# Optimization experiments

Hardware: AMD Instinct MI355X
Metric: run time of the kernel (lower is better)

## Reference

```python
import jax, jax.numpy as jnp
import numpy as np

N = 300000        # active voxels
C = 64            # channels (in_dim == out_dim)
K = 27            # 3x3x3 kernel offsets
EPS = 1e-5        # BatchNorm eps
GX, GY, GZ = 256, 256, 32  # voxel grid


def _build_neighbors():
    """Submanifold rulebook: for each active voxel, index of the active voxel at
    each of the 27 offsets, or -1 if that neighbor voxel is inactive."""
    rng = np.random.default_rng(0)
    lin = np.sort(rng.choice(GX * GY * GZ, size=N, replace=False))
    x, y, z = lin // (GY * GZ), (lin // GZ) % GY, lin % GZ
    nbr = np.full((N, K), -1, dtype=np.int32)
    k = 0
    for dx in (-1, 0, 1):
        for dy in (-1, 0, 1):
            for dz in (-1, 0, 1):
                nx, ny, nz = x + dx, y + dy, z + dz
                inb = (nx >= 0) & (nx < GX) & (ny >= 0) & (ny < GY) & (nz >= 0) & (nz < GZ)
                nl = (nx * GY + ny) * GZ + nz
                pos = np.searchsorted(lin, nl)
                posc = np.clip(pos, 0, N - 1)
                found = inb & (lin[posc] == nl)
                nbr[:, k] = np.where(found, posc, -1)
                k += 1
    return jnp.asarray(nbr)


def setup_inputs() -> dict:
    key = jax.random.key(0)
    k0, k1, k2 = jax.random.split(key, 3)
    return {
        "feats": jax.random.normal(k0, (N, C), dtype=jnp.float32),
        "W1": jax.random.normal(k1, (K, C, C), dtype=jnp.float32) * 0.05,
        "gamma1": jnp.ones((C,), jnp.float32),
        "beta1": jnp.zeros((C,), jnp.float32),
        "W2": jax.random.normal(k2, (K, C, C), dtype=jnp.float32) * 0.05,
        "gamma2": jnp.ones((C,), jnp.float32),
        "beta2": jnp.zeros((C,), jnp.float32),
        "neighbor_idx": _build_neighbors(),
    }


def _subm_conv(feats, W, nbr):
    # gather -> matmul -> accumulate, one pass per kernel offset (fixed K=27)
    mask = nbr >= 0
    idx = jnp.where(mask, nbr, 0)
    out = jnp.zeros((feats.shape[0], W.shape[-1]), feats.dtype)
    for k in range(K):
        g = feats[idx[:, k]] * mask[:, k:k + 1].astype(feats.dtype)  # [N, C]
        out = out + g @ W[k]
    return out


def _bn_relu(x, gamma, beta):
    # BatchNorm1d training-mode forward: biased batch stats over active voxels
    mu = jnp.mean(x, axis=0)
    var = jnp.var(x, axis=0)
    return jax.nn.relu((x - mu) * jax.lax.rsqrt(var + EPS) * gamma + beta)


def reference(feats, W1, gamma1, beta1, W2, gamma2, beta2, neighbor_idx):
    x_net = _bn_relu(_subm_conv(feats, W1, neighbor_idx), gamma1, beta1)
    res = _bn_relu(_subm_conv(x_net, W2, neighbor_idx), gamma2, beta2)
    return x_net + res
```

## Files before the change

### kernel.cpp

```cpp
#include <hip/hip_runtime.h>
#include <cstdint>
#include <cstddef>

typedef unsigned short u16;
typedef __bf16 bf16x8 __attribute__((ext_vector_type(8)));
typedef float f32x4 __attribute__((ext_vector_type(4)));

#define KOFF 27
#define EPSBN 1e-5f

__device__ inline u16 f2bf(float f) {
  unsigned int u = __float_as_uint(f);
  unsigned int r = (u + 0x7FFFu + ((u >> 16) & 1u)) >> 16;
  return (u16)r;
}
__device__ inline float bf2f(u16 h) {
  return __uint_as_float(((unsigned int)h) << 16);
}


__global__ void k_prep_feats(const float* __restrict__ in, u16* __restrict__ out,
                             float* __restrict__ stats, int n4) {
  if (blockIdx.x == 0) stats[threadIdx.x] = 0.f;
  int i = blockIdx.x * 256 + threadIdx.x;
  if (i >= n4) return;
  const float4 v = reinterpret_cast<const float4*>(in)[i];
  ushort4 o;
  o.x = f2bf(v.x); o.y = f2bf(v.y); o.z = f2bf(v.z); o.w = f2bf(v.w);
  reinterpret_cast<ushort4*>(out)[i] = o;
}

__global__ void k_prep_w(const float* __restrict__ W, u16* __restrict__ Wp) {
  int tid = blockIdx.x * 256 + threadIdx.x;
  if (tid >= KOFF * 4096) return;
  int k = tid >> 12;
  int rem = tid & 4095;
  int slot = rem >> 3;
  int e = rem & 7;
  int ks = slot >> 8;
  int ct = (slot >> 6) & 3;
  int lane = slot & 63;
  int j = ks * 32 + ((lane >> 4) << 3) + e;
  int c = ct * 16 + (lane & 15);
  Wp[tid] = f2bf(W[(k * 64 + j) * 64 + c]);
}

__global__ void k_prep_nbrT(const int* __restrict__ nbr, int* __restrict__ nbrT, int N) {
  __shared__ int L[64 * KOFF];
  const int t = threadIdx.x;
  const int v0 = blockIdx.x * 64;
  const int nv = min(64, N - v0);
  const int cnt = nv * KOFF;
  for (int i = t; i < cnt; i += 256) L[i] = nbr[(size_t)v0 * KOFF + i];
  __syncthreads();
  for (int i = t; i < KOFF * 64; i += 256) {
    int k = i >> 6, j = i & 63;
    if (j < nv) nbrT[(size_t)k * N + v0 + j] = L[j * KOFF + k];
  }
}

__launch_bounds__(256, 3)
__global__ void k_conv(const u16* __restrict__ F, const u16* __restrict__ Wp,
                       const int* __restrict__ nbrT, float* __restrict__ out,
                       float* __restrict__ stats, int N) {
  const int t = threadIdx.x;
  const int w = t >> 6;
  const int lane = t & 63;
  const int vbase = blockIdx.x * 256 + (w << 6) + (lane & 15);
  const int ch = (lane >> 4) << 3;

  f32x4 acc[4][4];
#pragma unroll
  for (int m = 0; m < 4; ++m)
#pragma unroll
    for (int c = 0; c < 4; ++c) acc[m][c] = (f32x4){0.f, 0.f, 0.f, 0.f};

  int nid[4];
#pragma unroll
  for (int m = 0; m < 4; ++m) {
    const int v = vbase + (m << 4);
    nid[m] = (v < N) ? nbrT[v] : -1;
  }

  const u16* bp = Wp + ((size_t)lane << 3);

#pragma unroll 3
  for (int k = 0; k < KOFF; ++k) {
    bf16x8 bfr[2][4];
#pragma unroll
    for (int ks = 0; ks < 2; ++ks)
#pragma unroll
      for (int c = 0; c < 4; ++c)
        bfr[ks][c] = *reinterpret_cast<const bf16x8*>(bp + ((size_t)k << 12) + (ks << 11) + (c << 9));

    bf16x8 a0[4], a1[4];
#pragma unroll
    for (int m = 0; m < 4; ++m) {
      a0[m] = (bf16x8){};
      a1[m] = (bf16x8){};
      const int id = nid[m];
      if (id >= 0) {
        const u16* fr = F + ((size_t)id << 6) + ch;
        a0[m] = *reinterpret_cast<const bf16x8*>(fr);
        a1[m] = *reinterpret_cast<const bf16x8*>(fr + 32);
      }
    }

    if (k + 1 < KOFF) {
      const int* nk = nbrT + (size_t)(k + 1) * N;
#pragma unroll
      for (int m = 0; m < 4; ++m) {
        const int v = vbase + (m << 4);
        nid[m] = (v < N) ? nk[v] : -1;
      }
    }

#pragma unroll
    for (int m = 0; m < 4; ++m)
#pragma unroll
      for (int c = 0; c < 4; ++c)
        acc[m][c] = __builtin_amdgcn_mfma_f32_16x16x32_bf16(a0[m], bfr[0][c], acc[m][c], 0, 0, 0);
#pragma unroll
    for (int m = 0; m < 4; ++m)
#pragma unroll
      for (int c = 0; c < 4; ++c)
        acc[m][c] = __builtin_amdgcn_mfma_f32_16x16x32_bf16(a1[m], bfr[1][c], acc[m][c], 0, 0, 0);
  }

  const int row0 = blockIdx.x * 256 + (w << 6) + ((lane >> 4) << 2);
#pragma unroll
  for (int m = 0; m < 4; ++m) {
#pragma unroll
    for (int c = 0; c < 4; ++c) {
      const int col = (c << 4) + (lane & 15);
#pragma unroll
      for (int e = 0; e < 4; ++e) {
        const int v = row0 + (m << 4) + e;
        if (v < N) out[((size_t)v << 6) + col] = acc[m][c][e];
      }
    }
  }

  __shared__ float sred[4][128];
#pragma unroll
  for (int c = 0; c < 4; ++c) {
    float s = 0.f, q = 0.f;
#pragma unroll
    for (int m = 0; m < 4; ++m)
#pragma unroll
      for (int e = 0; e < 4; ++e) {
        const float x = acc[m][c][e];
        s += x;
        q += x * x;
      }
    s += __shfl_xor(s, 16, 64);
    s += __shfl_xor(s, 32, 64);
    q += __shfl_xor(q, 16, 64);
    q += __shfl_xor(q, 32, 64);
    if (lane < 16) {
      sred[w][(c << 4) + lane] = s;
      sred[w][64 + (c << 4) + lane] = q;
    }
  }
  __syncthreads();
  if (t < 128) {
    const float tot = sred[0][t] + sred[1][t] + sred[2][t] + sred[3][t];
    atomicAdd(&stats[t], tot);
  }
}


__global__ void k_final(const float* __restrict__ stats, const float* __restrict__ gamma,
                        const float* __restrict__ beta, float* __restrict__ sb, int N) {
  const int c = threadIdx.x;
  const float inv = 1.0f / (float)N;
  const float mu = stats[c] * inv;
  const float var = stats[64 + c] * inv - mu * mu;
  const float sc = gamma[c] * rsqrtf(var + EPSBN);
  sb[c] = sc;
  sb[64 + c] = beta[c] - mu * sc;
}

__global__ void k_apply1(const float* __restrict__ x, const float* __restrict__ sb,
                         u16* __restrict__ xb, int n4) {
  int i = blockIdx.x * 256 + threadIdx.x;
  if (i >= n4) return;
  const int cg = i & 15;
  float4 v = reinterpret_cast<const float4*>(x)[i];
  const float4 sc = reinterpret_cast<const float4*>(sb)[cg];
  const float4 bi = reinterpret_cast<const float4*>(sb)[16 + cg];
  float y0 = fmaxf(0.f, v.x * sc.x + bi.x);
  float y1 = fmaxf(0.f, v.y * sc.y + bi.y);
  float y2 = fmaxf(0.f, v.z * sc.z + bi.z);
  float y3 = fmaxf(0.f, v.w * sc.w + bi.w);
  ushort4 o;
  o.x = f2bf(y0); o.y = f2bf(y1); o.z = f2bf(y2); o.w = f2bf(y3);
  reinterpret_cast<ushort4*>(xb)[i] = o;
}

__global__ void k_apply2(float* __restrict__ io, const float* __restrict__ sb,
                         const u16* __restrict__ xb, int n4) {
  int i = blockIdx.x * 256 + threadIdx.x;
  if (i >= n4) return;
  const int cg = i & 15;
  float4 v = reinterpret_cast<const float4*>(io)[i];
  const float4 sc = reinterpret_cast<const float4*>(sb)[cg];
  const float4 bi = reinterpret_cast<const float4*>(sb)[16 + cg];
  const ushort4 xn = reinterpret_cast<const ushort4*>(xb)[i];
  float4 o;
  o.x = bf2f(xn.x) + fmaxf(0.f, v.x * sc.x + bi.x);
  o.y = bf2f(xn.y) + fmaxf(0.f, v.y * sc.y + bi.y);
  o.z = bf2f(xn.z) + fmaxf(0.f, v.z * sc.z + bi.z);
  o.w = bf2f(xn.w) + fmaxf(0.f, v.w * sc.w + bi.w);
  reinterpret_cast<float4*>(io)[i] = o;
}


extern "C" void kernel_launch(void* const* d_in, const int* in_sizes, int n_in,
                              void* d_out, int out_size, void* d_ws, size_t ws_size,
                              hipStream_t stream) {
  const float* feats = (const float*)d_in[0];
  const float* W1 = (const float*)d_in[1];
  const float* g1 = (const float*)d_in[2];
  const float* b1 = (const float*)d_in[3];
  const float* W2 = (const float*)d_in[4];
  const float* g2 = (const float*)d_in[5];
  const float* b2 = (const float*)d_in[6];
  const int* nbr = (const int*)d_in[7];
  const int N = in_sizes[0] / 64;

  char* ws = (char*)d_ws;
  size_t off = 0;
  auto alloc = [&](size_t bytes) {
    void* p = ws + off;
    off = (off + bytes + 255) & ~(size_t)255;
    return p;
  };
  u16* featsb = (u16*)alloc((size_t)N * 64 * 2);
  u16* xnetb = (u16*)alloc((size_t)N * 64 * 2);
  u16* w1p = (u16*)alloc((size_t)KOFF * 4096 * 2);
  u16* w2p = (u16*)alloc((size_t)KOFF * 4096 * 2);
  float* stats = (float*)alloc(256 * 4);
  float* sb1 = (float*)alloc(128 * 4);
  float* sb2 = (float*)alloc(128 * 4);
  int* nbrT = (int*)alloc((size_t)KOFF * N * 4);
  float* outf = (float*)d_out;

  const int n4 = N * 16;
  const int gApply = (n4 + 255) / 256;
  const int gW = (KOFF * 4096 + 255) / 256;
  const int gConv = (N + 255) / 256;

  k_prep_feats<<<gApply, 256, 0, stream>>>(feats, featsb, stats, n4);
  k_prep_w<<<gW, 256, 0, stream>>>(W1, w1p);
  k_prep_w<<<gW, 256, 0, stream>>>(W2, w2p);
  k_prep_nbrT<<<(N + 63) / 64, 256, 0, stream>>>(nbr, nbrT, N);

  k_conv<<<gConv, 256, 0, stream>>>(featsb, w1p, nbrT, outf, stats, N);
  k_final<<<1, 64, 0, stream>>>(stats, g1, b1, sb1, N);
  k_apply1<<<gApply, 256, 0, stream>>>(outf, sb1, xnetb, n4);

  k_conv<<<gConv, 256, 0, stream>>>(xnetb, w2p, nbrT, outf, stats + 128, N);
  k_final<<<1, 64, 0, stream>>>(stats + 128, g2, b2, sb2, N);
  k_apply2<<<gApply, 256, 0, stream>>>(outf, sb2, xnetb, n4);
}
```

Baseline: 267.4 us.

## Double-buffer conv gathers, remap blocks per XCD, store raw conv outputs as bf16

The conv kernel now prefetches the next offset's neighbor features and weight fragments into a second register set while MFMAs run on the current set. It also skips MFMAs for 16-row groups whose neighbors are all missing, raises MFMA priority with s_setprio, and remaps block IDs so consecutive voxel tiles share an XCD's L2. Raw conv outputs are written as bf16 instead of fp32, which halves the write and re-read traffic in the apply kernels. The apply kernels are widened to 8 elements per thread. The costs are higher register pressure (occupancy hint lowered from 3 to 2) and extra bf16 rounding of the pre-BatchNorm values.

New measurement: 368.1 us. 1.38x slower.

```diff
diff --git a/kernel.cpp b/kernel.cpp
--- a/kernel.cpp
+++ b/kernel.cpp
@@ -59,15 +59,70 @@
   }
 }
 
-__launch_bounds__(256, 3)
+
+__device__ __forceinline__ void conv_step(
+    const u16* __restrict__ F, const u16* __restrict__ bp,
+    const int* __restrict__ nbrT, int N, int vbase, const bool (&vok)[4],
+    int kk, int chb,
+    bf16x8 (&c0)[4], bf16x8 (&c1)[4], bf16x8 (&cb)[2][4], bool (&cball)[4],
+    bf16x8 (&n0)[4], bf16x8 (&n1)[4], bf16x8 (&nb)[2][4], bool (&nball)[4],
+    int (&nid)[4], f32x4 (&acc)[4][4]) {
+  const int kn = kk + 1;
+  if (kn < KOFF) {
+#pragma unroll
+    for (int m = 0; m < 4; ++m) {
+      const int id = nid[m];
+      nball[m] = __any(id >= 0);
+      n0[m] = (bf16x8){};
+      n1[m] = (bf16x8){};
+      if (id >= 0) {
+        const char* fr = (const char*)F + ((size_t)(unsigned)id << 7) + chb;
+        n0[m] = *reinterpret_cast<const bf16x8*>(fr);
+        n1[m] = *reinterpret_cast<const bf16x8*>(fr + 64);
+      }
+    }
+    if (kn + 1 < KOFF) {
+      const int* nk = nbrT + (size_t)(kn + 1) * N + vbase;
+#pragma unroll
+      for (int m = 0; m < 4; ++m) nid[m] = vok[m] ? nk[m << 4] : -1;
+    }
+    const u16* bk = bp + ((size_t)kn << 12);
+#pragma unroll
+    for (int ks = 0; ks < 2; ++ks)
+#pragma unroll
+      for (int c = 0; c < 4; ++c)
+        nb[ks][c] = *reinterpret_cast<const bf16x8*>(bk + (ks << 11) + (c << 9));
+  }
+  __builtin_amdgcn_s_setprio(1);
+#pragma unroll
+  for (int m = 0; m < 4; ++m) {
+    if (cball[m]) {
+#pragma unroll
+      for (int c = 0; c < 4; ++c)
+        acc[m][c] = __builtin_amdgcn_mfma_f32_16x16x32_bf16(c0[m], cb[0][c], acc[m][c], 0, 0, 0);
+#pragma unroll
+      for (int c = 0; c < 4; ++c)
+        acc[m][c] = __builtin_amdgcn_mfma_f32_16x16x32_bf16(c1[m], cb[1][c], acc[m][c], 0, 0, 0);
+    }
+  }
+  __builtin_amdgcn_s_setprio(0);
+}
+
+__launch_bounds__(256, 2)
 __global__ void k_conv(const u16* __restrict__ F, const u16* __restrict__ Wp,
-                       const int* __restrict__ nbrT, float* __restrict__ out,
+                       const int* __restrict__ nbrT, u16* __restrict__ rawout,
                        float* __restrict__ stats, int N) {
   const int t = threadIdx.x;
   const int w = t >> 6;
   const int lane = t & 63;
-  const int vbase = blockIdx.x * 256 + (w << 6) + (lane & 15);
-  const int ch = (lane >> 4) << 3;
+
+  const int nwg = gridDim.x, bid = blockIdx.x;
+  const int q = nwg >> 3, r = nwg & 7;
+  const int xcd = bid & 7, o = bid >> 3;
+  const int wg = (xcd < r ? xcd * (q + 1) : r * (q + 1) + (xcd - r) * q) + o;
+
+  const int vbase = wg * 256 + (w << 6) + (lane & 15);
+  const int chb = (lane >> 4) << 4;
 
   f32x4 acc[4][4];
 #pragma unroll
@@ -75,59 +130,53 @@
 #pragma unroll
     for (int c = 0; c < 4; ++c) acc[m][c] = (f32x4){0.f, 0.f, 0.f, 0.f};
 
+  bool vok[4];
   int nid[4];
 #pragma unroll
   for (int m = 0; m < 4; ++m) {
     const int v = vbase + (m << 4);
-    nid[m] = (v < N) ? nbrT[v] : -1;
-  }
-
-  const u16* bp = Wp + ((size_t)lane << 3);
-
-#pragma unroll 3
-  for (int k = 0; k < KOFF; ++k) {
-    bf16x8 bfr[2][4];
-#pragma unroll
-    for (int ks = 0; ks < 2; ++ks)
-#pragma unroll
-      for (int c = 0; c < 4; ++c)
-        bfr[ks][c] = *reinterpret_cast<const bf16x8*>(bp + ((size_t)k << 12) + (ks << 11) + (c << 9));
-
-    bf16x8 a0[4], a1[4];
-#pragma unroll
-    for (int m = 0; m < 4; ++m) {
-      a0[m] = (bf16x8){};
-      a1[m] = (bf16x8){};
-      const int id = nid[m];
-      if (id >= 0) {
-        const u16* fr = F + ((size_t)id << 6) + ch;
-        a0[m] = *reinterpret_cast<const bf16x8*>(fr);
-        a1[m] = *reinterpret_cast<const bf16x8*>(fr + 32);
-      }
-    }
-
-    if (k + 1 < KOFF) {
-      const int* nk = nbrT + (size_t)(k + 1) * N;
-#pragma unroll
-      for (int m = 0; m < 4; ++m) {
-        const int v = vbase + (m << 4);
-        nid[m] = (v < N) ? nk[v] : -1;
-      }
-    }
-
-#pragma unroll
-    for (int m = 0; m < 4; ++m)
-#pragma unroll
-      for (int c = 0; c < 4; ++c)
-        acc[m][c] = __builtin_amdgcn_mfma_f32_16x16x32_bf16(a0[m], bfr[0][c], acc[m][c], 0, 0, 0);
-#pragma unroll
-    for (int m = 0; m < 4; ++m)
-#pragma unroll
-      for (int c = 0; c < 4; ++c)
-        acc[m][c] = __builtin_amdgcn_mfma_f32_16x16x32_bf16(a1[m], bfr[1][c], acc[m][c], 0, 0, 0);
-  }
-
-  const int row0 = blockIdx.x * 256 + (w << 6) + ((lane >> 4) << 2);
+    vok[m] = v < N;
+    nid[m] = vok[m] ? nbrT[v] : -1;
+  }
+
+  bf16x8 a0A[4], a1A[4], bA[2][4];
+  bf16x8 a0B[4], a1B[4], bB[2][4];
+  bool ballA[4], ballB[4];
+
+#pragma unroll
+  for (int m = 0; m < 4; ++m) {
+    const int id = nid[m];
+    ballA[m] = __any(id >= 0);
+    a0A[m] = (bf16x8){};
+    a1A[m] = (bf16x8){};
+    if (id >= 0) {
+      const char* fr = (const char*)F + ((size_t)(unsigned)id << 7) + chb;
+      a0A[m] = *reinterpret_cast<const bf16x8*>(fr);
+      a1A[m] = *reinterpret_cast<const bf16x8*>(fr + 64);
+    }
+  }
+  {
+    const int* nk = nbrT + (size_t)N + vbase;
+#pragma unroll
+    for (int m = 0; m < 4; ++m) nid[m] = vok[m] ? nk[m << 4] : -1;
+  }
+  const u16* bp = Wp + (lane << 3);
+#pragma unroll
+  for (int ks = 0; ks < 2; ++ks)
+#pragma unroll
+    for (int c = 0; c < 4; ++c)
+      bA[ks][c] = *reinterpret_cast<const bf16x8*>(bp + (ks << 11) + (c << 9));
+
+  for (int kb = 0; kb < 13; ++kb) {
+    conv_step(F, bp, nbrT, N, vbase, vok, 2 * kb, chb,
+              a0A, a1A, bA, ballA, a0B, a1B, bB, ballB, nid, acc);
+    conv_step(F, bp, nbrT, N, vbase, vok, 2 * kb + 1, chb,
+              a0B, a1B, bB, ballB, a0A, a1A, bA, ballA, nid, acc);
+  }
+  conv_step(F, bp, nbrT, N, vbase, vok, 26, chb,
+            a0A, a1A, bA, ballA, a0B, a1B, bB, ballB, nid, acc);
+
+  const int row0 = wg * 256 + (w << 6) + ((lane >> 4) << 2);
 #pragma unroll
   for (int m = 0; m < 4; ++m) {
 #pragma unroll
@@ -136,7 +185,7 @@
 #pragma unroll
       for (int e = 0; e < 4; ++e) {
         const int v = row0 + (m << 4) + e;
-        if (v < N) out[((size_t)v << 6) + col] = acc[m][c][e];
+        if (v < N) rawout[((size_t)v << 6) + col] = f2bf(acc[m][c][e]);
       }
     }
   }
@@ -144,22 +193,22 @@
   __shared__ float sred[4][128];
 #pragma unroll
   for (int c = 0; c < 4; ++c) {
-    float s = 0.f, q = 0.f;
+    float s = 0.f, qq = 0.f;
 #pragma unroll
     for (int m = 0; m < 4; ++m)
 #pragma unroll
       for (int e = 0; e < 4; ++e) {
         const float x = acc[m][c][e];
         s += x;
-        q += x * x;
+        qq += x * x;
       }
     s += __shfl_xor(s, 16, 64);
     s += __shfl_xor(s, 32, 64);
-    q += __shfl_xor(q, 16, 64);
-    q += __shfl_xor(q, 32, 64);
+    qq += __shfl_xor(qq, 16, 64);
+    qq += __shfl_xor(qq, 32, 64);
     if (lane < 16) {
       sred[w][(c << 4) + lane] = s;
-      sred[w][64 + (c << 4) + lane] = q;
+      sred[w][64 + (c << 4) + lane] = qq;
     }
   }
   __syncthreads();
@@ -181,38 +230,58 @@
   sb[64 + c] = beta[c] - mu * sc;
 }
 
-__global__ void k_apply1(const float* __restrict__ x, const float* __restrict__ sb,
-                         u16* __restrict__ xb, int n4) {
+__global__ void k_apply1(const u16* __restrict__ raw, const float* __restrict__ sb,
+                         u16* __restrict__ xb, int n8) {
   int i = blockIdx.x * 256 + threadIdx.x;
-  if (i >= n4) return;
-  const int cg = i & 15;
-  float4 v = reinterpret_cast<const float4*>(x)[i];
-  const float4 sc = reinterpret_cast<const float4*>(sb)[cg];
-  const float4 bi = reinterpret_cast<const float4*>(sb)[16 + cg];
-  float y0 = fmaxf(0.f, v.x * sc.x + bi.x);
-  float y1 = fmaxf(0.f, v.y * sc.y + bi.y);
-  float y2 = fmaxf(0.f, v.z * sc.z + bi.z);
-  float y3 = fmaxf(0.f, v.w * sc.w + bi.w);
-  ushort4 o;
-  o.x = f2bf(y0); o.y = f2bf(y1); o.z = f2bf(y2); o.w = f2bf(y3);
-  reinterpret_cast<ushort4*>(xb)[i] = o;
-}
-
-__global__ void k_apply2(float* __restrict__ io, const float* __restrict__ sb,
-                         const u16* __restrict__ xb, int n4) {
+  if (i >= n8) return;
+  const int cg = (i & 7) << 1;
+  const uint4 rv = reinterpret_cast<const uint4*>(raw)[i];
+  const float4 s0 = reinterpret_cast<const float4*>(sb)[cg];
+  const float4 s1 = reinterpret_cast<const float4*>(sb)[cg + 1];
+  const float4 b0 = reinterpret_cast<const float4*>(sb + 64)[cg];
+  const float4 b1 = reinterpret_cast<const float4*>(sb + 64)[cg + 1];
+  uint4 ov;
+  {
+    float y0 = fmaxf(0.f, bf2f((u16)(rv.x & 0xffff)) * s0.x + b0.x);
+    float y1 = fmaxf(0.f, bf2f((u16)(rv.x >> 16)) * s0.y + b0.y);
+    float y2 = fmaxf(0.f, bf2f((u16)(rv.y & 0xffff)) * s0.z + b0.z);
+    float y3 = fmaxf(0.f, bf2f((u16)(rv.y >> 16)) * s0.w + b0.w);
+    ov.x = (unsigned)f2bf(y0) | ((unsigned)f2bf(y1) << 16);
+    ov.y = (unsigned)f2bf(y2) | ((unsigned)f2bf(y3) << 16);
+  }
+  {
+    float y0 = fmaxf(0.f, bf2f((u16)(rv.z & 0xffff)) * s1.x + b1.x);
+    float y1 = fmaxf(0.f, bf2f((u16)(rv.z >> 16)) * s1.y + b1.y);
+    float y2 = fmaxf(0.f, bf2f((u16)(rv.w & 0xffff)) * s1.z + b1.z);
+    float y3 = fmaxf(0.f, bf2f((u16)(rv.w >> 16)) * s1.w + b1.w);
+    ov.z = (unsigned)f2bf(y0) | ((unsigned)f2bf(y1) << 16);
+    ov.w = (unsigned)f2bf(y2) | ((unsigned)f2bf(y3) << 16);
+  }
+  reinterpret_cast<uint4*>(xb)[i] = ov;
+}
+
+__global__ void k_apply2(const u16* __restrict__ raw, const float* __restrict__ sb,
+                         const u16* __restrict__ xb, float* __restrict__ out, int n8) {
   int i = blockIdx.x * 256 + threadIdx.x;
-  if (i >= n4) return;
-  const int cg = i & 15;
-  float4 v = reinterpret_cast<const float4*>(io)[i];
-  const float4 sc = reinterpret_cast<const float4*>(sb)[cg];
-  const float4 bi = reinterpret_cast<const float4*>(sb)[16 + cg];
-  const ushort4 xn = reinterpret_cast<const ushort4*>(xb)[i];
-  float4 o;
-  o.x = bf2f(xn.x) + fmaxf(0.f, v.x * sc.x + bi.x);
-  o.y = bf2f(xn.y) + fmaxf(0.f, v.y * sc.y + bi.y);
-  o.z = bf2f(xn.z) + fmaxf(0.f, v.z * sc.z + bi.z);
-  o.w = bf2f(xn.w) + fmaxf(0.f, v.w * sc.w + bi.w);
-  reinterpret_cast<float4*>(io)[i] = o;
+  if (i >= n8) return;
+  const int cg = (i & 7) << 1;
+  const uint4 rv = reinterpret_cast<const uint4*>(raw)[i];
+  const uint4 xv = reinterpret_cast<const uint4*>(xb)[i];
+  const float4 s0 = reinterpret_cast<const float4*>(sb)[cg];
+  const float4 s1 = reinterpret_cast<const float4*>(sb)[cg + 1];
+  const float4 b0 = reinterpret_cast<const float4*>(sb + 64)[cg];
+  const float4 b1 = reinterpret_cast<const float4*>(sb + 64)[cg + 1];
+  float4 o0, o1;
+  o0.x = bf2f((u16)(xv.x & 0xffff)) + fmaxf(0.f, bf2f((u16)(rv.x & 0xffff)) * s0.x + b0.x);
+  o0.y = bf2f((u16)(xv.x >> 16)) + fmaxf(0.f, bf2f((u16)(rv.x >> 16)) * s0.y + b0.y);
+  o0.z = bf2f((u16)(xv.y & 0xffff)) + fmaxf(0.f, bf2f((u16)(rv.y & 0xffff)) * s0.z + b0.z);
+  o0.w = bf2f((u16)(xv.y >> 16)) + fmaxf(0.f, bf2f((u16)(rv.y >> 16)) * s0.w + b0.w);
+  o1.x = bf2f((u16)(xv.z & 0xffff)) + fmaxf(0.f, bf2f((u16)(rv.z & 0xffff)) * s1.x + b1.x);
+  o1.y = bf2f((u16)(xv.z >> 16)) + fmaxf(0.f, bf2f((u16)(rv.z >> 16)) * s1.y + b1.y);
+  o1.z = bf2f((u16)(xv.w & 0xffff)) + fmaxf(0.f, bf2f((u16)(rv.w & 0xffff)) * s1.z + b1.z);
+  o1.w = bf2f((u16)(xv.w >> 16)) + fmaxf(0.f, bf2f((u16)(rv.w >> 16)) * s1.w + b1.w);
+  reinterpret_cast<float4*>(out)[2 * i] = o0;
+  reinterpret_cast<float4*>(out)[2 * i + 1] = o1;
 }
 
 
@@ -244,23 +313,28 @@
   float* sb1 = (float*)alloc(128 * 4);
   float* sb2 = (float*)alloc(128 * 4);
   int* nbrT = (int*)alloc((size_t)KOFF * N * 4);
+
+  u16* raw1 = (u16*)d_out;
+  u16* raw2 = featsb;
   float* outf = (float*)d_out;
 
   const int n4 = N * 16;
-  const int gApply = (n4 + 255) / 256;
+  const int n8 = N * 8;
+  const int gPrep = (n4 + 255) / 256;
+  const int gApply = (n8 + 255) / 256;
   const int gW = (KOFF * 4096 + 255) / 256;
   const int gConv = (N + 255) / 256;
 
-  k_prep_feats<<<gApply, 256, 0, stream>>>(feats, featsb, stats, n4);
+  k_prep_feats<<<gPrep, 256, 0, stream>>>(feats, featsb, stats, n4);
   k_prep_w<<<gW, 256, 0, stream>>>(W1, w1p);
   k_prep_w<<<gW, 256, 0, stream>>>(W2, w2p);
   k_prep_nbrT<<<(N + 63) / 64, 256, 0, stream>>>(nbr, nbrT, N);
 
-  k_conv<<<gConv, 256, 0, stream>>>(featsb, w1p, nbrT, outf, stats, N);
+  k_conv<<<gConv, 256, 0, stream>>>(featsb, w1p, nbrT, raw1, stats, N);
   k_final<<<1, 64, 0, stream>>>(stats, g1, b1, sb1, N);
-  k_apply1<<<gApply, 256, 0, stream>>>(outf, sb1, xnetb, n4);
-
-  k_conv<<<gConv, 256, 0, stream>>>(xnetb, w2p, nbrT, outf, stats + 128, N);
+  k_apply1<<<gApply, 256, 0, stream>>>(raw1, sb1, xnetb, n8);
+
+  k_conv<<<gConv, 256, 0, stream>>>(xnetb, w2p, nbrT, raw2, stats + 128, N);
   k_final<<<1, 64, 0, stream>>>(stats + 128, g2, b2, sb2, N);
-  k_apply2<<<gApply, 256, 0, stream>>>(outf, sb2, xnetb, n4);
-}
+  k_apply2<<<gApply, 256, 0, stream>>>(raw2, sb2, xnetb, outf, n8);
+}
```

## Halve conv tile per block, raise occupancy, remap blocks across XCDs

Applied to the files above, without the earlier changes.

The conv kernel now processes 128 voxels per block instead of 256, with 2 M-tiles per wave instead of 4. This cuts accumulator registers and allows 4 blocks per SIMD set via launch bounds. Block IDs are remapped so that consecutive voxel ranges land on the same XCD, which should improve L2 locality for neighbor gathers. The cost is that each B-fragment weight load is reused across fewer MFMAs, raising weight-load traffic per voxel.

After: 324.8 us. 1.21x slower.

```diff
diff --git a/kernel.cpp b/kernel.cpp
--- a/kernel.cpp
+++ b/kernel.cpp
@@ -59,30 +59,38 @@
   }
 }
 
-__launch_bounds__(256, 3)
+__launch_bounds__(256, 4)
 __global__ void k_conv(const u16* __restrict__ F, const u16* __restrict__ Wp,
                        const int* __restrict__ nbrT, float* __restrict__ out,
                        float* __restrict__ stats, int N) {
   const int t = threadIdx.x;
   const int w = t >> 6;
   const int lane = t & 63;
-  const int vbase = blockIdx.x * 256 + (w << 6) + (lane & 15);
+
+  const int nwg = gridDim.x, bid = blockIdx.x;
+  const int q = nwg >> 3, r = nwg & 7;
+  const int xcd = bid & 7, o = bid >> 3;
+  const int wg = (xcd < r ? xcd * (q + 1) : r * (q + 1) + (xcd - r) * q) + o;
+
+  const int vbase = wg * 128 + (w << 5) + (lane & 15);
   const int ch = (lane >> 4) << 3;
 
-  f32x4 acc[4][4];
-#pragma unroll
-  for (int m = 0; m < 4; ++m)
+  f32x4 acc[2][4];
+#pragma unroll
+  for (int m = 0; m < 2; ++m)
 #pragma unroll
     for (int c = 0; c < 4; ++c) acc[m][c] = (f32x4){0.f, 0.f, 0.f, 0.f};
 
-  int nid[4];
-#pragma unroll
-  for (int m = 0; m < 4; ++m) {
+  bool vok[2];
+  int nid[2];
+#pragma unroll
+  for (int m = 0; m < 2; ++m) {
     const int v = vbase + (m << 4);
-    nid[m] = (v < N) ? nbrT[v] : -1;
-  }
-
-  const u16* bp = Wp + ((size_t)lane << 3);
+    vok[m] = v < N;
+    nid[m] = vok[m] ? nbrT[v] : -1;
+  }
+
+  const u16* bp = Wp + (lane << 3);
 
 #pragma unroll 3
   for (int k = 0; k < KOFF; ++k) {
@@ -93,14 +101,14 @@
       for (int c = 0; c < 4; ++c)
         bfr[ks][c] = *reinterpret_cast<const bf16x8*>(bp + ((size_t)k << 12) + (ks << 11) + (c << 9));
 
-    bf16x8 a0[4], a1[4];
-#pragma unroll
-    for (int m = 0; m < 4; ++m) {
+    bf16x8 a0[2], a1[2];
+#pragma unroll
+    for (int m = 0; m < 2; ++m) {
       a0[m] = (bf16x8){};
       a1[m] = (bf16x8){};
       const int id = nid[m];
       if (id >= 0) {
-        const u16* fr = F + ((size_t)id << 6) + ch;
+        const u16* fr = F + ((size_t)(unsigned)id << 6) + ch;
         a0[m] = *reinterpret_cast<const bf16x8*>(fr);
         a1[m] = *reinterpret_cast<const bf16x8*>(fr + 32);
       }
@@ -109,27 +117,27 @@
     if (k + 1 < KOFF) {
       const int* nk = nbrT + (size_t)(k + 1) * N;
 #pragma unroll
-      for (int m = 0; m < 4; ++m) {
+      for (int m = 0; m < 2; ++m) {
         const int v = vbase + (m << 4);
         nid[m] = (v < N) ? nk[v] : -1;
       }
     }
 
 #pragma unroll
-    for (int m = 0; m < 4; ++m)
+    for (int m = 0; m < 2; ++m)
 #pragma unroll
       for (int c = 0; c < 4; ++c)
         acc[m][c] = __builtin_amdgcn_mfma_f32_16x16x32_bf16(a0[m], bfr[0][c], acc[m][c], 0, 0, 0);
 #pragma unroll
-    for (int m = 0; m < 4; ++m)
+    for (int m = 0; m < 2; ++m)
 #pragma unroll
       for (int c = 0; c < 4; ++c)
         acc[m][c] = __builtin_amdgcn_mfma_f32_16x16x32_bf16(a1[m], bfr[1][c], acc[m][c], 0, 0, 0);
   }
 
-  const int row0 = blockIdx.x * 256 + (w << 6) + ((lane >> 4) << 2);
-#pragma unroll
-  for (int m = 0; m < 4; ++m) {
+  const int row0 = wg * 128 + (w << 5) + ((lane >> 4) << 2);
+#pragma unroll
+  for (int m = 0; m < 2; ++m) {
 #pragma unroll
     for (int c = 0; c < 4; ++c) {
       const int col = (c << 4) + (lane & 15);
@@ -144,22 +152,22 @@
   __shared__ float sred[4][128];
 #pragma unroll
   for (int c = 0; c < 4; ++c) {
-    float s = 0.f, q = 0.f;
-#pragma unroll
-    for (int m = 0; m < 4; ++m)
+    float s = 0.f, qq = 0.f;
+#pragma unroll
+    for (int m = 0; m < 2; ++m)
 #pragma unroll
       for (int e = 0; e < 4; ++e) {
         const float x = acc[m][c][e];
         s += x;
-        q += x * x;
+        qq += x * x;
       }
     s += __shfl_xor(s, 16, 64);
     s += __shfl_xor(s, 32, 64);
-    q += __shfl_xor(q, 16, 64);
-    q += __shfl_xor(q, 32, 64);
+    qq += __shfl_xor(qq, 16, 64);
+    qq += __shfl_xor(qq, 32, 64);
     if (lane < 16) {
       sred[w][(c << 4) + lane] = s;
-      sred[w][64 + (c << 4) + lane] = q;
+      sred[w][64 + (c << 4) + lane] = qq;
     }
   }
   __syncthreads();
@@ -247,20 +255,20 @@
   float* outf = (float*)d_out;
 
   const int n4 = N * 16;
-  const int gApply = (n4 + 255) / 256;
+  const int gPrep = (n4 + 255) / 256;
   const int gW = (KOFF * 4096 + 255) / 256;
-  const int gConv = (N + 255) / 256;
-
-  k_prep_feats<<<gApply, 256, 0, stream>>>(feats, featsb, stats, n4);
+  const int gConv = (N + 127) / 128;
+
+  k_prep_feats<<<gPrep, 256, 0, stream>>>(feats, featsb, stats, n4);
   k_prep_w<<<gW, 256, 0, stream>>>(W1, w1p);
   k_prep_w<<<gW, 256, 0, stream>>>(W2, w2p);
   k_prep_nbrT<<<(N + 63) / 64, 256, 0, stream>>>(nbr, nbrT, N);
 
   k_conv<<<gConv, 256, 0, stream>>>(featsb, w1p, nbrT, outf, stats, N);
   k_final<<<1, 64, 0, stream>>>(stats, g1, b1, sb1, N);
-  k_apply1<<<gApply, 256, 0, stream>>>(outf, sb1, xnetb, n4);
+  k_apply1<<<gPrep, 256, 0, stream>>>(outf, sb1, xnetb, n4);
 
   k_conv<<<gConv, 256, 0, stream>>>(xnetb, w2p, nbrT, outf, stats + 128, N);
   k_final<<<1, 64, 0, stream>>>(stats + 128, g2, b2, sb2, N);
-  k_apply2<<<gApply, 256, 0, stream>>>(outf, sb2, xnetb, n4);
-}
+  k_apply2<<<gPrep, 256, 0, stream>>>(outf, sb2, xnetb, n4);
+}
```

## Software-pipeline conv gathers, pack neighbor indices, remap blocks per XCD, fuse prep kernels

Applied to the files above, without the earlier changes.

Restructures the conv main loop so the next offset's feature gathers are issued in between the two MFMA halves, using setprio to favour matrix work. Neighbor indices are repacked as int4 per 16-lane group with a sentinel row, so one vector load fetches all four rows' ids. Block ids are remapped so consecutive voxel groups land on the same XCD, which should improve L2 locality for neighbor gathers. The three prep kernels are merged into one launch. Risks are higher register pressure from the extra live fragments and a larger index buffer.

Result: slower. 292.7 us (+9.5%).

```diff
diff --git a/kernel.cpp b/kernel.cpp
--- a/kernel.cpp
+++ b/kernel.cpp
@@ -18,56 +18,82 @@
   return __uint_as_float(((unsigned int)h) << 16);
 }
 
-
-__global__ void k_prep_feats(const float* __restrict__ in, u16* __restrict__ out,
-                             float* __restrict__ stats, int n4) {
-  if (blockIdx.x == 0) stats[threadIdx.x] = 0.f;
-  int i = blockIdx.x * 256 + threadIdx.x;
+__global__ void k_prep(const float* __restrict__ feats, const float* __restrict__ W1,
+                       const float* __restrict__ W2, const int* __restrict__ nbr,
+                       u16* __restrict__ featsb, u16* __restrict__ w1p,
+                       u16* __restrict__ w2p, int4* __restrict__ nbrP,
+                       float* __restrict__ stats, int N, int G, int gW, int n4) {
+  __shared__ int L[64 * KOFF];
+  const int t = threadIdx.x;
+  const int bid = blockIdx.x;
+
+  if (bid < G) {
+    const int g = bid;
+    const int v0 = g * 64;
+    for (int i = t; i < 64 * KOFF; i += 256) {
+      const int v = v0 + i / KOFF;
+      L[i] = (v < N) ? nbr[(size_t)v * KOFF + i % KOFF] : -1;
+    }
+    __syncthreads();
+    for (int i = t; i < KOFF * 16; i += 256) {
+      const int k = i >> 4, l = i & 15;
+      int4 val;
+      val.x = L[l * KOFF + k];
+      val.y = L[(l + 16) * KOFF + k];
+      val.z = L[(l + 32) * KOFF + k];
+      val.w = L[(l + 48) * KOFF + k];
+      nbrP[((size_t)k * G + g) * 16 + l] = val;
+    }
+    if (t < 16) nbrP[((size_t)KOFF * G + g) * 16 + t] = make_int4(-1, -1, -1, -1);
+    return;
+  }
+  if (bid < G + 2 * gW) {
+    const int wi = bid - G;
+    const bool second = wi >= gW;
+    const float* W = second ? W2 : W1;
+    u16* Wp = second ? w2p : w1p;
+    const int tid = (second ? wi - gW : wi) * 256 + t;
+    if (tid >= KOFF * 4096) return;
+    const int k = tid >> 12;
+    const int rem = tid & 4095;
+    const int slot = rem >> 3;
+    const int e = rem & 7;
+    const int ks = slot >> 8;
+    const int ct = (slot >> 6) & 3;
+    const int lane = slot & 63;
+    const int j = ks * 32 + ((lane >> 4) << 3) + e;
+    const int c = ct * 16 + (lane & 15);
+    Wp[tid] = f2bf(W[(k * 64 + j) * 64 + c]);
+    return;
+  }
+  const int idx = bid - G - 2 * gW;
+  if (idx == 0) stats[t] = 0.f;
+  const int i = idx * 256 + t;
   if (i >= n4) return;
-  const float4 v = reinterpret_cast<const float4*>(in)[i];
+  const float4 v = reinterpret_cast<const float4*>(feats)[i];
   ushort4 o;
   o.x = f2bf(v.x); o.y = f2bf(v.y); o.z = f2bf(v.z); o.w = f2bf(v.w);
-  reinterpret_cast<ushort4*>(out)[i] = o;
-}
-
-__global__ void k_prep_w(const float* __restrict__ W, u16* __restrict__ Wp) {
-  int tid = blockIdx.x * 256 + threadIdx.x;
-  if (tid >= KOFF * 4096) return;
-  int k = tid >> 12;
-  int rem = tid & 4095;
-  int slot = rem >> 3;
-  int e = rem & 7;
-  int ks = slot >> 8;
-  int ct = (slot >> 6) & 3;
-  int lane = slot & 63;
-  int j = ks * 32 + ((lane >> 4) << 3) + e;
-  int c = ct * 16 + (lane & 15);
-  Wp[tid] = f2bf(W[(k * 64 + j) * 64 + c]);
-}
-
-__global__ void k_prep_nbrT(const int* __restrict__ nbr, int* __restrict__ nbrT, int N) {
-  __shared__ int L[64 * KOFF];
-  const int t = threadIdx.x;
-  const int v0 = blockIdx.x * 64;
-  const int nv = min(64, N - v0);
-  const int cnt = nv * KOFF;
-  for (int i = t; i < cnt; i += 256) L[i] = nbr[(size_t)v0 * KOFF + i];
-  __syncthreads();
-  for (int i = t; i < KOFF * 64; i += 256) {
-    int k = i >> 6, j = i & 63;
-    if (j < nv) nbrT[(size_t)k * N + v0 + j] = L[j * KOFF + k];
-  }
+  reinterpret_cast<ushort4*>(featsb)[i] = o;
 }
 
 __launch_bounds__(256, 3)
 __global__ void k_conv(const u16* __restrict__ F, const u16* __restrict__ Wp,
-                       const int* __restrict__ nbrT, float* __restrict__ out,
-                       float* __restrict__ stats, int N) {
+                       const int4* __restrict__ nbrP, float* __restrict__ out,
+                       float* __restrict__ stats, int N, int G) {
+  __shared__ float sred[4][128];
   const int t = threadIdx.x;
   const int w = t >> 6;
   const int lane = t & 63;
-  const int vbase = blockIdx.x * 256 + (w << 6) + (lane & 15);
+
+  const int nwg = gridDim.x, bid = blockIdx.x;
+  const int q = nwg >> 3, r = nwg & 7;
+  const int xcd = bid & 7, o = bid >> 3;
+  const int wg = (xcd < r ? xcd * (q + 1) : r * (q + 1) + (xcd - r) * q) + o;
+
+  const int g = wg * 4 + w;
   const int ch = (lane >> 4) << 3;
+  const size_t G16 = (size_t)G * 16;
+  const int4* nb = nbrP + (size_t)g * 16 + (lane & 15);
 
   f32x4 acc[4][4];
 #pragma unroll
@@ -75,59 +101,91 @@
 #pragma unroll
     for (int c = 0; c < 4; ++c) acc[m][c] = (f32x4){0.f, 0.f, 0.f, 0.f};
 
-  int nid[4];
-#pragma unroll
-  for (int m = 0; m < 4; ++m) {
-    const int v = vbase + (m << 4);
-    nid[m] = (v < N) ? nbrT[v] : -1;
-  }
-
-  const u16* bp = Wp + ((size_t)lane << 3);
-
-#pragma unroll 3
-  for (int k = 0; k < KOFF; ++k) {
-    bf16x8 bfr[2][4];
-#pragma unroll
-    for (int ks = 0; ks < 2; ++ks)
-#pragma unroll
-      for (int c = 0; c < 4; ++c)
-        bfr[ks][c] = *reinterpret_cast<const bf16x8*>(bp + ((size_t)k << 12) + (ks << 11) + (c << 9));
-
-    bf16x8 a0[4], a1[4];
+  int4 idv = nb[0];
+  bf16x8 a0[4], a1[4];
+  {
+    const int ids[4] = {idv.x, idv.y, idv.z, idv.w};
 #pragma unroll
     for (int m = 0; m < 4; ++m) {
       a0[m] = (bf16x8){};
       a1[m] = (bf16x8){};
-      const int id = nid[m];
-      if (id >= 0) {
-        const u16* fr = F + ((size_t)id << 6) + ch;
+      if (ids[m] >= 0) {
+        const u16* fr = F + ((size_t)(unsigned)ids[m] << 6) + ch;
         a0[m] = *reinterpret_cast<const bf16x8*>(fr);
         a1[m] = *reinterpret_cast<const bf16x8*>(fr + 32);
       }
     }
-
-    if (k + 1 < KOFF) {
-      const int* nk = nbrT + (size_t)(k + 1) * N;
-#pragma unroll
-      for (int m = 0; m < 4; ++m) {
-        const int v = vbase + (m << 4);
-        nid[m] = (v < N) ? nk[v] : -1;
-      }
-    }
-
+  }
+  idv = nb[G16];
+
+  const u16* bp = Wp + (lane << 3);
+
+#pragma unroll 2
+  for (int k = 0; k < 26; ++k) {
+    bf16x8 bfr[2][4];
+    {
+      const u16* bk = bp + ((size_t)k << 12);
+#pragma unroll
+      for (int ks = 0; ks < 2; ++ks)
+#pragma unroll
+        for (int c = 0; c < 4; ++c)
+          bfr[ks][c] = *reinterpret_cast<const bf16x8*>(bk + (ks << 11) + (c << 9));
+    }
+    const int ids[4] = {idv.x, idv.y, idv.z, idv.w};
+    __builtin_amdgcn_s_setprio(1);
 #pragma unroll
     for (int m = 0; m < 4; ++m)
 #pragma unroll
       for (int c = 0; c < 4; ++c)
         acc[m][c] = __builtin_amdgcn_mfma_f32_16x16x32_bf16(a0[m], bfr[0][c], acc[m][c], 0, 0, 0);
+    __builtin_amdgcn_s_setprio(0);
+#pragma unroll
+    for (int m = 0; m < 4; ++m) {
+      bf16x8 v = (bf16x8){};
+      if (ids[m] >= 0)
+        v = *reinterpret_cast<const bf16x8*>(F + ((size_t)(unsigned)ids[m] << 6) + ch);
+      a0[m] = v;
+    }
+    __builtin_amdgcn_s_setprio(1);
 #pragma unroll
     for (int m = 0; m < 4; ++m)
 #pragma unroll
       for (int c = 0; c < 4; ++c)
         acc[m][c] = __builtin_amdgcn_mfma_f32_16x16x32_bf16(a1[m], bfr[1][c], acc[m][c], 0, 0, 0);
-  }
-
-  const int row0 = blockIdx.x * 256 + (w << 6) + ((lane >> 4) << 2);
+    __builtin_amdgcn_s_setprio(0);
+#pragma unroll
+    for (int m = 0; m < 4; ++m) {
+      bf16x8 v = (bf16x8){};
+      if (ids[m] >= 0)
+        v = *reinterpret_cast<const bf16x8*>(F + ((size_t)(unsigned)ids[m] << 6) + ch + 32);
+      a1[m] = v;
+    }
+    idv = nb[(size_t)(k + 2) * G16];
+  }
+
+  {
+    bf16x8 bfr[2][4];
+    const u16* bk = bp + ((size_t)26 << 12);
+#pragma unroll
+    for (int ks = 0; ks < 2; ++ks)
+#pragma unroll
+      for (int c = 0; c < 4; ++c)
+        bfr[ks][c] = *reinterpret_cast<const bf16x8*>(bk + (ks << 11) + (c << 9));
+    __builtin_amdgcn_s_setprio(1);
+#pragma unroll
+    for (int m = 0; m < 4; ++m)
+#pragma unroll
+      for (int c = 0; c < 4; ++c)
+        acc[m][c] = __builtin_amdgcn_mfma_f32_16x16x32_bf16(a0[m], bfr[0][c], acc[m][c], 0, 0, 0);
+#pragma unroll
+    for (int m = 0; m < 4; ++m)
+#pragma unroll
+      for (int c = 0; c < 4; ++c)
+        acc[m][c] = __builtin_amdgcn_mfma_f32_16x16x32_bf16(a1[m], bfr[1][c], acc[m][c], 0, 0, 0);
+    __builtin_amdgcn_s_setprio(0);
+  }
+
+  const int row0 = g * 64 + ((lane >> 4) << 2);
 #pragma unroll
   for (int m = 0; m < 4; ++m) {
 #pragma unroll
@@ -141,25 +199,24 @@
     }
   }
 
-  __shared__ float sred[4][128];
 #pragma unroll
   for (int c = 0; c < 4; ++c) {
-    float s = 0.f, q = 0.f;
+    float s = 0.f, qq = 0.f;
 #pragma unroll
     for (int m = 0; m < 4; ++m)
 #pragma unroll
       for (int e = 0; e < 4; ++e) {
         const float x = acc[m][c][e];
         s += x;
-        q += x * x;
+        qq += x * x;
       }
     s += __shfl_xor(s, 16, 64);
     s += __shfl_xor(s, 32, 64);
-    q += __shfl_xor(q, 16, 64);
-    q += __shfl_xor(q, 32, 64);
+    qq += __shfl_xor(qq, 16, 64);
+    qq += __shfl_xor(qq, 32, 64);
     if (lane < 16) {
       sred[w][(c << 4) + lane] = s;
-      sred[w][64 + (c << 4) + lane] = q;
+      sred[w][64 + (c << 4) + lane] = qq;
     }
   }
   __syncthreads();
@@ -228,6 +285,7 @@
   const float* b2 = (const float*)d_in[6];
   const int* nbr = (const int*)d_in[7];
   const int N = in_sizes[0] / 64;
+  const int G = (N + 63) / 64;
 
   char* ws = (char*)d_ws;
   size_t off = 0;
@@ -243,24 +301,22 @@
   float* stats = (float*)alloc(256 * 4);
   float* sb1 = (float*)alloc(128 * 4);
   float* sb2 = (float*)alloc(128 * 4);
-  int* nbrT = (int*)alloc((size_t)KOFF * N * 4);
+  int4* nbrP = (int4*)alloc((size_t)(KOFF + 1) * G * 16 * 16);
   float* outf = (float*)d_out;
 
   const int n4 = N * 16;
-  const int gApply = (n4 + 255) / 256;
+  const int gPrep = (n4 + 255) / 256;
   const int gW = (KOFF * 4096 + 255) / 256;
-  const int gConv = (N + 255) / 256;
-
-  k_prep_feats<<<gApply, 256, 0, stream>>>(feats, featsb, stats, n4);
-  k_prep_w<<<gW, 256, 0, stream>>>(W1, w1p);
-  k_prep_w<<<gW, 256, 0, stream>>>(W2, w2p);
-  k_prep_nbrT<<<(N + 63) / 64, 256, 0, stream>>>(nbr, nbrT, N);
-
-  k_conv<<<gConv, 256, 0, stream>>>(featsb, w1p, nbrT, outf, stats, N);
+  const int gConv = (G + 3) / 4;
+
+  k_prep<<<G + 2 * gW + gPrep, 256, 0, stream>>>(feats, W1, W2, nbr, featsb, w1p, w2p,
+                                                 nbrP, stats, N, G, gW, n4);
+
+  k_conv<<<gConv, 256, 0, stream>>>(featsb, w1p, nbrP, outf, stats, N, G);
   k_final<<<1, 64, 0, stream>>>(stats, g1, b1, sb1, N);
-  k_apply1<<<gApply, 256, 0, stream>>>(outf, sb1, xnetb, n4);
-
-  k_conv<<<gConv, 256, 0, stream>>>(xnetb, w2p, nbrT, outf, stats + 128, N);
+  k_apply1<<<gPrep, 256, 0, stream>>>(outf, sb1, xnetb, n4);
+
+  k_conv<<<gConv, 256, 0, stream>>>(xnetb, w2p, nbrP, outf, stats + 128, N, G);
   k_final<<<1, 64, 0, stream>>>(stats + 128, g2, b2, sb2, N);
-  k_apply2<<<gApply, 256, 0, stream>>>(outf, sb2, xnetb, n4);
-}
+  k_apply2<<<gPrep, 256, 0, stream>>>(outf, sb2, xnetb, n4);
+}
```
